# Performance work log

Measured on AMD Instinct MI355X. Metric: run time of the kernel, lower is better.

The kernel has to match this reference:

```python
import jax, jax.numpy as jnp
import numpy as np

N_HEAD, D_MODEL, D_HEAD = 16, 1024, 64
QLEN, BSZ, RLEN = 2048, 2, 2048
SCALE = 1.0 / (D_HEAD ** 0.5)


def setup_inputs() -> dict:
    key = jax.random.key(0)
    ks = jax.random.split(key, 7)
    return {
        "w": jax.random.normal(ks[0], (QLEN, BSZ, D_MODEL), dtype=jnp.float32),
        "r": jax.random.normal(ks[1], (RLEN, D_MODEL), dtype=jnp.float32),
        "qkv_w": jax.random.normal(ks[2], (D_MODEL, 3 * N_HEAD * D_HEAD), dtype=jnp.float32) * 0.02,
        "r_net_w": jax.random.normal(ks[3], (D_MODEL, N_HEAD * D_HEAD), dtype=jnp.float32) * 0.02,
        "o_w": jax.random.normal(ks[4], (N_HEAD * D_HEAD, D_MODEL), dtype=jnp.float32) * 0.02,
        "r_r_bias": jax.random.normal(ks[5], (N_HEAD, D_HEAD), dtype=jnp.float32) * 0.02,
        "r_w_bias": jax.random.normal(ks[6], (N_HEAD, D_HEAD), dtype=jnp.float32) * 0.02,
    }


def _rel_shift(x):
    # x: [qlen, rlen, bsz, n_head]
    q, r, b, n = x.shape
    x = jnp.pad(x, ((0, 0), (1, 0), (0, 0), (0, 0)))
    x = x.reshape(r + 1, q, b, n)[1:]
    return x.reshape(q, r, b, n)


def reference(w, r, qkv_w, r_net_w, o_w, r_r_bias, r_w_bias):
    qlen, bsz, _ = w.shape
    rlen = r.shape[0]
    # qkv projection: [qlen, bsz, 3*H*D]
    w_heads = jnp.einsum('ibm,mh->ibh', w, qkv_w)
    w_head_q, w_head_k, w_head_v = jnp.split(w_heads, 3, axis=-1)
    klen = w_head_k.shape[0]
    w_head_q = w_head_q.reshape(qlen, bsz, N_HEAD, D_HEAD)
    w_head_k = w_head_k.reshape(klen, bsz, N_HEAD, D_HEAD)
    w_head_v = w_head_v.reshape(klen, bsz, N_HEAD, D_HEAD)
    # relative position keys: [rlen, H, D]
    r_head_k = jnp.einsum('jm,mh->jh', r, r_net_w).reshape(rlen, N_HEAD, D_HEAD)

    rw_head_q = w_head_q + r_w_bias  # content bias
    rr_head_q = w_head_q + r_r_bias  # position bias
    AC = jnp.einsum('ibnd,jbnd->ijbn', rw_head_q, w_head_k)
    BD = jnp.einsum('ibnd,jnd->ijbn', rr_head_q, r_head_k)
    BD = _rel_shift(BD)[:, :klen]

    attn_score = (AC + BD) * SCALE
    attn_prob = jax.nn.softmax(attn_score, axis=1)  # over klen axis
    attn_vec = jnp.einsum('ijbn,jbnd->ibnd', attn_prob, w_head_v)
    attn_vec = attn_vec.reshape(qlen, bsz, N_HEAD * D_HEAD)
    attn_out = jnp.einsum('ibh,hm->ibm', attn_vec, o_w)
    return (w + attn_out, attn_prob, AC, BD)
```

## Files before the change

kernel.cpp:

```cpp
#include <hip/hip_runtime.h>
#include <hip/hip_bf16.h>


typedef unsigned short u16;
typedef __attribute__((ext_vector_type(8))) short short8;
typedef __attribute__((ext_vector_type(4))) float f32x4;
typedef __attribute__((ext_vector_type(4))) unsigned short u16x4;

__device__ __forceinline__ u16 f2bf(float x){
  unsigned u = __float_as_uint(x);
  u += 0x7fffu + ((u >> 16) & 1u);
  return (u16)(u >> 16);
}
__device__ __forceinline__ float bf2f(u16 s){
  return __uint_as_float(((unsigned)s) << 16);
}
__device__ __forceinline__ f32x4 mfma16(short8 a, short8 b, f32x4 c){
  return __builtin_amdgcn_mfma_f32_16x16x32_bf16(a, b, c, 0, 0, 0);
}
__device__ __forceinline__ void ntst4(float* p, f32x4 v){
  __builtin_nontemporal_store(v, (f32x4*)p);
}
__device__ __forceinline__ void bar_lds(){
  asm volatile("s_waitcnt lgkmcnt(0)" ::: "memory");
  __builtin_amdgcn_s_barrier();
}


__global__ __launch_bounds__(256) void k_cast(const float* __restrict__ src, u16* __restrict__ dst, int n4){
  int i = blockIdx.x * 256 + threadIdx.x;
  if (i >= n4) return;
  f32x4 v = *(const f32x4*)(src + (size_t)i * 4);
  u16x4 o;
  #pragma unroll
  for (int q = 0; q < 4; ++q) o[q] = f2bf(v[q]);
  *(u16x4*)(dst + (size_t)i * 4) = o;
}

__global__ __launch_bounds__(256) void k_tc(const float* __restrict__ src, u16* __restrict__ dst, int R, int C){
  __shared__ float ld[32][33];
  int c0 = blockIdx.x * 32, r0 = blockIdx.y * 32;
  int t = threadIdx.x;
  int r = t >> 3, c4 = (t & 7) * 4;
  f32x4 v = *(const f32x4*)(src + (size_t)(r0 + r) * C + c0 + c4);
  #pragma unroll
  for (int q = 0; q < 4; ++q) ld[r][c4 + q] = v[q];
  __syncthreads();
  int c = t >> 3, r4 = (t & 7) * 4;
  u16x4 o;
  #pragma unroll
  for (int q = 0; q < 4; ++q) o[q] = f2bf(ld[r4 + q][c]);
  *(u16x4*)(dst + (size_t)(c0 + c) * R + r0 + r4) = o;
}


template<int MODE>
__global__ __launch_bounds__(512) void k_gemm(const u16* __restrict__ A, const u16* __restrict__ Bt,
        u16* __restrict__ o0, u16* __restrict__ o1, u16* __restrict__ o2,
        const float* __restrict__ wres, float* __restrict__ outf)
{
  __shared__ __align__(16) u16 As[128][40];
  __shared__ __align__(16) u16 Bs[256][40];
  const int t = threadIdx.x;
  const int wave = t >> 6, lane = t & 63;
  const int wr = wave >> 2, wc = wave & 3;
  const int g = lane >> 4, li = lane & 15;
  const int m0 = blockIdx.x * 128, n0 = blockIdx.y * 256;
  f32x4 acc[4][4] = {};
  const int ar = t >> 2, ac8 = (t & 3) * 8;
  for (int kt = 0; kt < 32; ++kt){
    int k0 = kt * 32;
    *(short8*)&As[ar][ac8] = *(const short8*)(A + (size_t)(m0 + ar) * 1024 + k0 + ac8);
    #pragma unroll
    for (int u = 0; u < 2; ++u){
      int id = t + 512 * u; int br = id >> 2, bc8 = (id & 3) * 8;
      *(short8*)&Bs[br][bc8] = *(const short8*)(Bt + (size_t)(n0 + br) * 1024 + k0 + bc8);
    }
    bar_lds();
    short8 af[4], bfv[4];
    #pragma unroll
    for (int mf = 0; mf < 4; ++mf) af[mf] = *(const short8*)&As[wr * 64 + mf * 16 + li][g * 8];
    #pragma unroll
    for (int nf = 0; nf < 4; ++nf) bfv[nf] = *(const short8*)&Bs[wc * 64 + nf * 16 + li][g * 8];
    #pragma unroll
    for (int mf = 0; mf < 4; ++mf)
      #pragma unroll
      for (int nf = 0; nf < 4; ++nf)
        acc[mf][nf] = mfma16(af[mf], bfv[nf], acc[mf][nf]);
    bar_lds();
  }
  #pragma unroll
  for (int mf = 0; mf < 4; ++mf)
  #pragma unroll
  for (int nf = 0; nf < 4; ++nf)
  #pragma unroll
  for (int r = 0; r < 4; ++r){
    int gr = m0 + wr * 64 + mf * 16 + g * 4 + r;
    int gc = n0 + wc * 64 + nf * 16 + li;
    float v = acc[mf][nf][r];
    if (MODE == 0){
      int part = gc >> 10, hh = gc & 1023;
      int hn = hh >> 6, d = hh & 63;
      int i = gr >> 1, b = gr & 1;
      u16* dst = (part == 0) ? o0 : ((part == 1) ? o1 : o2);
      dst[((((b << 4) + hn) * 2048 + i) << 6) + d] = f2bf(v);
    } else if (MODE == 1){
      int hn = gc >> 6, d = gc & 63;
      o0[((hn * 2048 + gr) << 6) + d] = f2bf(v);
    } else {
      size_t idx = (size_t)gr * 1024 + gc;
      outf[idx] = wres[idx] + v;
    }
  }
}

__global__ __launch_bounds__(256) void k_bias(const u16* __restrict__ Km, const float* __restrict__ bv,
                                              float* __restrict__ out, int total){
  int idx = blockIdx.x * 256 + threadIdx.x;
  if (idx >= total) return;
  int n = (idx >> 11) & 15;
  const u16* kr = Km + ((size_t)idx << 6);
  const float* bp = bv + n * 64;
  float s = 0.f;
  #pragma unroll
  for (int d8 = 0; d8 < 8; ++d8){
    short8 v = *(const short8*)(kr + d8 * 8);
    #pragma unroll
    for (int q = 0; q < 8; ++q) s += bp[d8 * 8 + q] * bf2f((u16)v[q]);
  }
  out[idx] = s;
}

__global__ __launch_bounds__(256) void k_trv(const u16* __restrict__ V, u16* __restrict__ Vt){
  __shared__ __align__(16) u16 ld[64][72];
  int bn = blockIdx.x, j0 = blockIdx.y * 64;
  int t = threadIdx.x;
  #pragma unroll
  for (int u = 0; u < 2; ++u){
    int id = t + 256 * u; int r = id >> 3, c8 = (id & 7) * 8;
    *(short8*)&ld[r][c8] = *(const short8*)(V + ((size_t)(bn * 2048 + j0 + r) << 6) + c8);
  }
  __syncthreads();
  #pragma unroll
  for (int u = 0; u < 2; ++u){
    int id = t + 256 * u; int d = id >> 3, j8 = (id & 7) * 8;
    short8 o;
    #pragma unroll
    for (int q = 0; q < 8; ++q) o[q] = ld[j8 + q][d];
    *(short8*)(Vt + ((size_t)(bn * 64 + d) << 11) + j0 + j8) = o;
  }
}

template<typename F>
__device__ __forceinline__ void ring_step(int ch, int m, F&& do_tile){
  if (ch == 0){
    do_tile(m + 2032, false);
    do_tile(m - 32, true);
    do_tile(m - 16, true);
  }
  do_tile(m + 2048, false);
  do_tile(m + 2064, false);
  do_tile(m, true);
  do_tile(m + 16, true);
}

__global__ __launch_bounds__(512, 4) void k_statsR(const u16* __restrict__ Q, const u16* __restrict__ RK,
        const u16* __restrict__ Kc, const float* __restrict__ bias_ac, const float* __restrict__ bias_bd,
        float* __restrict__ ACo, float* __restrict__ BDo,
        float* __restrict__ m_part, float* __restrict__ l_part)
{
  __shared__ u16 sBD[2][16 * 544];
  __shared__ u16 sB[32 * 271];
  const int t = threadIdx.x, wave = t >> 6, lane = t & 63;
  const int g = lane >> 4, li = lane & 15;
  const int i0 = blockIdx.x * 16, b = blockIdx.y;
  const int jbase = blockIdx.z * 512;
  short8 qa[2][2], qb[2][2];
  #pragma unroll
  for (int nn = 0; nn < 2; ++nn){
    int bn = b * 16 + wave * 2 + nn;
    const u16* qp = Q + ((size_t)(bn * 2048 + i0 + li) << 6) + g * 8;
    qa[nn][0] = *(const short8*)qp;
    qa[nn][1] = *(const short8*)(qp + 32);
    int rowB = i0 + 1 + li; if (rowB > 2047) rowB = 2047;
    const u16* qp2 = Q + ((size_t)(bn * 2048 + rowB) << 6) + g * 8;
    qb[nn][0] = *(const short8*)qp2;
    qb[nn][1] = *(const short8*)(qp2 + 32);
  }
  for (int w2 = t; w2 < 2 * 4352; w2 += 512) ((unsigned*)sBD)[w2] = 0;

  float m_[2][4], l_[2][4];
  #pragma unroll
  for (int nn = 0; nn < 2; ++nn)
    #pragma unroll
    for (int r = 0; r < 4; ++r){ m_[nn][r] = -__builtin_inff(); l_[nn][r] = 0.f; }

  int cur = 0;
  for (int ch = 0; ch < 16; ++ch){
    int j0 = jbase + ch * 32;
    int m = j0 - i0;
    bar_lds();
    u16* bufA = &sBD[cur][0];
    u16* bufB = &sBD[cur ^ 1][0];

    auto do_tile = [&](int c0, bool case2){
      if (c0 < 0 || c0 > 2032) return;
      int off = c0 - m + (case2 ? 2 : -2047);
      #pragma unroll
      for (int nn = 0; nn < 2; ++nn){
        int n = wave * 2 + nn;
        const u16* rp = RK + ((size_t)(n * 2048 + c0 + li) << 6) + g * 8;
        short8 b0 = *(const short8*)rp;
        short8 b1 = *(const short8*)(rp + 32);
        f32x4 acc = {};
        acc = mfma16(case2 ? qb[nn][0] : qa[nn][0], b0, acc);
        acc = mfma16(case2 ? qb[nn][1] : qa[nn][1], b1, acc);
        float bb = bias_bd[n * 2048 + c0 + li];
        #pragma unroll
        for (int r = 0; r < 4; ++r){
          int fr = g * 4 + r;
          int jw = li + fr + off;
          u16 val = f2bf(acc[r] + bb);
          if ((unsigned)jw < 32u)       bufA[fr * 544 + jw * 17 + n] = val;
          else if ((unsigned)jw < 64u)  bufB[fr * 544 + (jw - 32) * 17 + n] = val;
        }
      }
    };
    ring_step(ch, m, do_tile);
    bar_lds();

    #pragma unroll
    for (int nn = 0; nn < 2; ++nn){
      int n = wave * 2 + nn, bn = b * 16 + n;
      float sv[2][4];
      #pragma unroll
      for (int cf = 0; cf < 2; ++cf){
        int jc = j0 + cf * 16 + li;
        const u16* kp = Kc + ((size_t)(bn * 2048 + jc) << 6) + g * 8;
        short8 b0 = *(const short8*)kp;
        short8 b1 = *(const short8*)(kp + 32);
        f32x4 acc = {};
        acc = mfma16(qa[nn][0], b0, acc);
        acc = mfma16(qa[nn][1], b1, acc);
        float ba = bias_ac[bn * 2048 + jc];
        #pragma unroll
        for (int r = 0; r < 4; ++r){
          float av = acc[r] + ba;
          sB[(cf * 16 + li) * 271 + n * 17 + g * 4 + r] = f2bf(av);
          float bd = bf2f(bufA[(g * 4 + r) * 544 + (cf * 16 + li) * 17 + n]);
          sv[cf][r] = (av + bd) * 0.125f;
        }
      }
      float cm[4], mn[4], ps[4];
      #pragma unroll
      for (int r = 0; r < 4; ++r) cm[r] = fmaxf(sv[0][r], sv[1][r]);
      #pragma unroll
      for (int off = 1; off < 16; off <<= 1)
        #pragma unroll
        for (int r = 0; r < 4; ++r) cm[r] = fmaxf(cm[r], __shfl_xor(cm[r], off));
      #pragma unroll
      for (int r = 0; r < 4; ++r){
        mn[r] = fmaxf(m_[nn][r], cm[r]);
        ps[r] = __expf(sv[0][r] - mn[r]) + __expf(sv[1][r] - mn[r]);
      }
      #pragma unroll
      for (int off = 1; off < 16; off <<= 1)
        #pragma unroll
        for (int r = 0; r < 4; ++r) ps[r] += __shfl_xor(ps[r], off);
      #pragma unroll
      for (int r = 0; r < 4; ++r){
        l_[nn][r] = l_[nn][r] * __expf(m_[nn][r] - mn[r]) + ps[r];
        m_[nn][r] = mn[r];
      }
    }
    #pragma unroll
    for (int u = 0; u < 4; ++u){
      int flat4 = t + 512 * u;
      int n4 = (flat4 & 3) * 4, jl = (flat4 >> 2) & 31, row = flat4 >> 7;
      f32x4 v;
      #pragma unroll
      for (int q = 0; q < 4; ++q) v[q] = bf2f(bufA[row * 544 + jl * 17 + n4 + q]);
      ntst4(BDo + (((size_t)(i0 + row) * 2048 + j0 + jl) << 5) + b * 16 + n4, v);
    }
    bar_lds();
    #pragma unroll
    for (int u = 0; u < 4; ++u){
      int flat4 = t + 512 * u;
      int n4 = (flat4 & 3) * 4, jl = (flat4 >> 2) & 31, row = flat4 >> 7;
      f32x4 v;
      #pragma unroll
      for (int q = 0; q < 4; ++q) v[q] = bf2f(sB[jl * 271 + (n4 + q) * 17 + row]);
      ntst4(ACo + (((size_t)(i0 + row) * 2048 + j0 + jl) << 5) + b * 16 + n4, v);
    }
    for (int w2 = t; w2 < 4352; w2 += 512) ((unsigned*)bufA)[w2] = 0;
    cur ^= 1;
  }
  if (li == 0){
    #pragma unroll
    for (int nn = 0; nn < 2; ++nn)
      #pragma unroll
      for (int r = 0; r < 4; ++r){
        int bn = b * 16 + wave * 2 + nn;
        size_t o = ((size_t)(blockIdx.z * 32 + bn)) * 2048 + i0 + g * 4 + r;
        m_part[o] = m_[nn][r];
        l_part[o] = l_[nn][r];
      }
  }
}

__global__ __launch_bounds__(256) void k_comb(const float* __restrict__ mp, const float* __restrict__ lp,
                                              float* __restrict__ mf, float* __restrict__ lf){
  int idx = blockIdx.x * 256 + threadIdx.x;
  float m = -__builtin_inff();
  #pragma unroll
  for (int js = 0; js < 4; ++js) m = fmaxf(m, mp[js * 65536 + idx]);
  float l = 0.f;
  #pragma unroll
  for (int js = 0; js < 4; ++js) l += lp[js * 65536 + idx] * __expf(mp[js * 65536 + idx] - m);
  mf[idx] = m;
  lf[idx] = l;
}

__global__ __launch_bounds__(512, 4) void k_prob_pv(const u16* __restrict__ Q, const u16* __restrict__ Kc,
        const u16* __restrict__ Vt, const float* __restrict__ bias_ac, const float* __restrict__ BD,
        const float* __restrict__ m_f, const float* __restrict__ l_f,
        float* __restrict__ PROB, float* __restrict__ Ovp)
{
  __shared__ __align__(16) u16 sA[16 * 648];
  __shared__ u16 sB[32 * 271];
  const int t = threadIdx.x, wave = t >> 6, lane = t & 63;
  const int g = lane >> 4, li = lane & 15;
  const int i0 = blockIdx.x * 16, b = blockIdx.y;
  const int jbase = blockIdx.z * 512;
  short8 qa[2][2];
  float m_[2][4], rl_[2][4];
  #pragma unroll
  for (int nn = 0; nn < 2; ++nn){
    int bn = b * 16 + wave * 2 + nn;
    const u16* qp = Q + ((size_t)(bn * 2048 + i0 + li) << 6) + g * 8;
    qa[nn][0] = *(const short8*)qp;
    qa[nn][1] = *(const short8*)(qp + 32);
    #pragma unroll
    for (int r = 0; r < 4; ++r){
      m_[nn][r]  = m_f[bn * 2048 + i0 + g * 4 + r];
      rl_[nn][r] = 1.f / l_f[bn * 2048 + i0 + g * 4 + r];
    }
  }
  f32x4 oacc[2][4] = {};

  f32x4 pfv[4];
  #pragma unroll
  for (int u = 0; u < 4; ++u){
    int flat4 = t + 512 * u;
    int n4 = (flat4 & 3) * 4, jl = (flat4 >> 2) & 31, row = flat4 >> 7;
    pfv[u] = *(const f32x4*)(BD + (((size_t)(i0 + row) * 2048 + jbase + jl) << 5) + b * 16 + n4);
  }

  for (int ch = 0; ch < 16; ++ch){
    int j0 = jbase + ch * 32;
    bar_lds();
    #pragma unroll
    for (int u = 0; u < 4; ++u){
      int flat4 = t + 512 * u;
      int n4 = (flat4 & 3) * 4, jl = (flat4 >> 2) & 31, row = flat4 >> 7;
      u16x4 o;
      #pragma unroll
      for (int q = 0; q < 4; ++q) o[q] = (u16)(__float_as_uint(pfv[u][q]) >> 16);
      *(u16x4*)&sA[row * 648 + jl * 20 + n4] = o;
    }
    if (ch + 1 < 16){
      #pragma unroll
      for (int u = 0; u < 4; ++u){
        int flat4 = t + 512 * u;
        int n4 = (flat4 & 3) * 4, jl = (flat4 >> 2) & 31, row = flat4 >> 7;
        pfv[u] = *(const f32x4*)(BD + (((size_t)(i0 + row) * 2048 + j0 + 32 + jl) << 5) + b * 16 + n4);
      }
    }
    bar_lds();
    #pragma unroll
    for (int nn = 0; nn < 2; ++nn){
      int n = wave * 2 + nn, bn = b * 16 + n;
      #pragma unroll
      for (int cf = 0; cf < 2; ++cf){
        int jc = j0 + cf * 16 + li;
        const u16* kp = Kc + ((size_t)(bn * 2048 + jc) << 6) + g * 8;
        short8 b0 = *(const short8*)kp;
        short8 b1 = *(const short8*)(kp + 32);
        f32x4 acc = {};
        acc = mfma16(qa[nn][0], b0, acc);
        acc = mfma16(qa[nn][1], b1, acc);
        float ba = bias_ac[bn * 2048 + jc];
        #pragma unroll
        for (int r = 0; r < 4; ++r){
          float bd = bf2f(sA[(g * 4 + r) * 648 + (cf * 16 + li) * 20 + n]);
          float s = (acc[r] + ba + bd) * 0.125f;
          float p = __expf(s - m_[nn][r]) * rl_[nn][r];
          sB[(cf * 16 + li) * 271 + n * 17 + g * 4 + r] = f2bf(p);
        }
      }
    }
    #pragma unroll
    for (int nn = 0; nn < 2; ++nn){
      int n = wave * 2 + nn, bn = b * 16 + n;
      short8 pa;
      #pragma unroll
      for (int tt = 0; tt < 8; ++tt) pa[tt] = (short)sB[(g * 8 + tt) * 271 + n * 17 + li];
      const u16* vb = Vt + ((size_t)(bn * 64) << 11) + j0 + g * 8;
      #pragma unroll
      for (int vf = 0; vf < 4; ++vf){
        short8 bv = *(const short8*)(vb + ((size_t)(vf * 16 + li) << 11));
        oacc[nn][vf] = mfma16(pa, bv, oacc[nn][vf]);
      }
    }
    bar_lds();
    #pragma unroll
    for (int u = 0; u < 4; ++u){
      int flat4 = t + 512 * u;
      int n4 = (flat4 & 3) * 4, jl = (flat4 >> 2) & 31, row = flat4 >> 7;
      f32x4 v;
      #pragma unroll
      for (int q = 0; q < 4; ++q) v[q] = bf2f(sB[jl * 271 + (n4 + q) * 17 + row]);
      ntst4(PROB + (((size_t)(i0 + row) * 2048 + j0 + jl) << 5) + b * 16 + n4, v);
    }
  }
  float* op = Ovp + (size_t)blockIdx.z * 4194304;
  #pragma unroll
  for (int nn = 0; nn < 2; ++nn){
    int n = wave * 2 + nn;
    #pragma unroll
    for (int vf = 0; vf < 4; ++vf)
      #pragma unroll
      for (int r = 0; r < 4; ++r)
        op[(size_t)((i0 + g * 4 + r) * 2 + b) * 1024 + n * 64 + vf * 16 + li] = oacc[nn][vf][r];
  }
}

__global__ __launch_bounds__(256) void k_ovred(const float* __restrict__ ovp, u16* __restrict__ ov){
  int i = blockIdx.x * 256 + threadIdx.x;
  const f32x4* p = (const f32x4*)ovp;
  f32x4 s = p[i];
  #pragma unroll
  for (int js = 1; js < 4; ++js) s += p[(size_t)js * 1048576 + i];
  u16x4 o;
  #pragma unroll
  for (int q = 0; q < 4; ++q) o[q] = f2bf(s[q]);
  ((u16x4*)ov)[i] = o;
}


extern "C" void kernel_launch(void* const* d_in, const int* in_sizes, int n_in,
                              void* d_out, int out_size, void* d_ws, size_t ws_size,
                              hipStream_t stream)
{
  const float* w      = (const float*)d_in[0];
  const float* r      = (const float*)d_in[1];
  const float* qkv_w  = (const float*)d_in[2];
  const float* rnet_w = (const float*)d_in[3];
  const float* o_w    = (const float*)d_in[4];
  const float* rrb    = (const float*)d_in[5];
  const float* rwb    = (const float*)d_in[6];

  char* ws = (char*)d_ws;
  size_t off = 0;
  auto alloc = [&](size_t bytes) -> void* {
    void* p = ws + off; off += (bytes + 255) & ~(size_t)255; return p;
  };
  u16* Xbf    = (u16*)alloc((size_t)4096 * 1024 * 2);
  u16* Rbf    = (u16*)alloc((size_t)2048 * 1024 * 2);
  u16* Wqkvt  = (u16*)alloc((size_t)3072 * 1024 * 2);
  u16* Wrt    = (u16*)alloc((size_t)1024 * 1024 * 2);
  u16* Wot    = (u16*)alloc((size_t)1024 * 1024 * 2);
  u16* Qs     = (u16*)alloc((size_t)32 * 2048 * 64 * 2);
  u16* Ks     = (u16*)alloc((size_t)32 * 2048 * 64 * 2);
  u16* Vs     = (u16*)alloc((size_t)32 * 2048 * 64 * 2);
  u16* Vts    = (u16*)alloc((size_t)32 * 64 * 2048 * 2);
  u16* RKs    = (u16*)alloc((size_t)16 * 2048 * 64 * 2);
  float* bias_ac = (float*)alloc((size_t)32 * 2048 * 4);
  float* bias_bd = (float*)alloc((size_t)16 * 2048 * 4);
  float* m_part  = (float*)alloc((size_t)4 * 32 * 2048 * 4);
  float* l_part  = (float*)alloc((size_t)4 * 32 * 2048 * 4);
  float* m_fin   = (float*)alloc((size_t)32 * 2048 * 4);
  float* l_fin   = (float*)alloc((size_t)32 * 2048 * 4);
  float* Ovp     = (float*)alloc((size_t)4 * 4096 * 1024 * 4);
  u16* Ov     = (u16*)alloc((size_t)4096 * 1024 * 2);

  float* out0 = (float*)d_out;
  float* PROB = out0 + 4194304;
  float* ACo  = PROB + 134217728;
  float* BDo  = ACo  + 134217728;

  k_cast<<<dim3(4096), dim3(256), 0, stream>>>(w, Xbf, 1048576);
  k_cast<<<dim3(2048), dim3(256), 0, stream>>>(r, Rbf, 524288);
  k_tc<<<dim3(96, 32), dim3(256), 0, stream>>>(qkv_w,  Wqkvt, 1024, 3072);
  k_tc<<<dim3(32, 32), dim3(256), 0, stream>>>(rnet_w, Wrt,   1024, 1024);
  k_tc<<<dim3(32, 32), dim3(256), 0, stream>>>(o_w,    Wot,   1024, 1024);
  k_gemm<0><<<dim3(32, 12), dim3(512), 0, stream>>>(Xbf, Wqkvt, Qs, Ks, Vs, nullptr, nullptr);
  k_gemm<1><<<dim3(16, 4),  dim3(512), 0, stream>>>(Rbf, Wrt,  RKs, nullptr, nullptr, nullptr, nullptr);
  k_bias<<<dim3(256), dim3(256), 0, stream>>>(Ks,  rwb, bias_ac, 65536);
  k_bias<<<dim3(128), dim3(256), 0, stream>>>(RKs, rrb, bias_bd, 32768);
  k_trv<<<dim3(32, 32), dim3(256), 0, stream>>>(Vs, Vts);
  k_statsR<<<dim3(128, 2, 4), dim3(512), 0, stream>>>(Qs, RKs, Ks, bias_ac, bias_bd, ACo, BDo, m_part, l_part);
  k_comb<<<dim3(256), dim3(256), 0, stream>>>(m_part, l_part, m_fin, l_fin);
  k_prob_pv<<<dim3(128, 2, 4), dim3(512), 0, stream>>>(Qs, Ks, Vts, bias_ac, BDo, m_fin, l_fin, PROB, Ovp);
  k_ovred<<<dim3(4096), dim3(256), 0, stream>>>(Ovp, Ov);
  k_gemm<2><<<dim3(32, 4), dim3(512), 0, stream>>>(Ov, Wot, nullptr, nullptr, nullptr, w, out0);
}
```

Baseline: 1.243 ms.

## Recompute BD in prob pass instead of rereading it, swap MFMA operands

The probability/PV kernel now recomputes the relative-position BD scores through the same ring-buffered MFMA scheme as the stats kernel, instead of reading the fp32 BD output back from global memory. Both kernels swap MFMA operand order so each lane holds one query row, which turns per-row softmax reductions into scalar values with two cross-lane shuffles. They also use vectorized bias loads, an XOR-swizzled LDS layout and packed P fragments built straight from registers. This trades a large global read for extra MFMA work and LDS ring maintenance in the second pass.

```diff
diff --git a/kernel.cpp b/kernel.cpp
--- a/kernel.cpp
+++ b/kernel.cpp
@@ -4,6 +4,7 @@
 
 typedef unsigned short u16;
 typedef __attribute__((ext_vector_type(8))) short short8;
+typedef __attribute__((ext_vector_type(4))) short s16x4;
 typedef __attribute__((ext_vector_type(4))) float f32x4;
 typedef __attribute__((ext_vector_type(4))) unsigned short u16x4;
 
@@ -24,6 +25,9 @@
 __device__ __forceinline__ void bar_lds(){
   asm volatile("s_waitcnt lgkmcnt(0)" ::: "memory");
   __builtin_amdgcn_s_barrier();
+}
+__device__ __forceinline__ int ridx(int il, int k, int n){
+  return (((il * 8 + k) << 4) + n) ^ (il & 15);
 }
 
 
@@ -76,7 +80,7 @@
       int id = t + 512 * u; int br = id >> 2, bc8 = (id & 3) * 8;
       *(short8*)&Bs[br][bc8] = *(const short8*)(Bt + (size_t)(n0 + br) * 1024 + k0 + bc8);
     }
-    bar_lds();
+    __syncthreads();
     short8 af[4], bfv[4];
     #pragma unroll
     for (int mf = 0; mf < 4; ++mf) af[mf] = *(const short8*)&As[wr * 64 + mf * 16 + li][g * 8];
@@ -87,7 +91,7 @@
       #pragma unroll
       for (int nf = 0; nf < 4; ++nf)
         acc[mf][nf] = mfma16(af[mf], bfv[nf], acc[mf][nf]);
-    bar_lds();
+    __syncthreads();
   }
   #pragma unroll
   for (int mf = 0; mf < 4; ++mf)
@@ -169,8 +173,8 @@
         float* __restrict__ ACo, float* __restrict__ BDo,
         float* __restrict__ m_part, float* __restrict__ l_part)
 {
-  __shared__ u16 sBD[2][16 * 544];
-  __shared__ u16 sB[32 * 271];
+  __shared__ __align__(16) u16 sRing[2][8192];
+  __shared__ __align__(16) u16 sAC[8192];
   const int t = threadIdx.x, wave = t >> 6, lane = t & 63;
   const int g = lane >> 4, li = lane & 15;
   const int i0 = blockIdx.x * 16, b = blockIdx.y;
@@ -187,21 +191,19 @@
     qb[nn][0] = *(const short8*)qp2;
     qb[nn][1] = *(const short8*)(qp2 + 32);
   }
-  for (int w2 = t; w2 < 2 * 4352; w2 += 512) ((unsigned*)sBD)[w2] = 0;
-
-  float m_[2][4], l_[2][4];
-  #pragma unroll
-  for (int nn = 0; nn < 2; ++nn)
-    #pragma unroll
-    for (int r = 0; r < 4; ++r){ m_[nn][r] = -__builtin_inff(); l_[nn][r] = 0.f; }
+  for (int w2 = t; w2 < 8192; w2 += 512) ((unsigned*)sRing)[w2] = 0;
+
+  float m_[2], l_[2];
+  #pragma unroll
+  for (int nn = 0; nn < 2; ++nn){ m_[nn] = -__builtin_inff(); l_[nn] = 0.f; }
 
   int cur = 0;
   for (int ch = 0; ch < 16; ++ch){
     int j0 = jbase + ch * 32;
     int m = j0 - i0;
     bar_lds();
-    u16* bufA = &sBD[cur][0];
-    u16* bufB = &sBD[cur ^ 1][0];
+    u16* bufA = &sRing[cur][0];
+    u16* bufB = &sRing[cur ^ 1][0];
 
     auto do_tile = [&](int c0, bool case2){
       if (c0 < 0 || c0 > 2032) return;
@@ -213,16 +215,15 @@
         short8 b0 = *(const short8*)rp;
         short8 b1 = *(const short8*)(rp + 32);
         f32x4 acc = {};
-        acc = mfma16(case2 ? qb[nn][0] : qa[nn][0], b0, acc);
-        acc = mfma16(case2 ? qb[nn][1] : qa[nn][1], b1, acc);
-        float bb = bias_bd[n * 2048 + c0 + li];
+        acc = mfma16(b0, case2 ? qb[nn][0] : qa[nn][0], acc);
+        acc = mfma16(b1, case2 ? qb[nn][1] : qa[nn][1], acc);
+        f32x4 bb4 = *(const f32x4*)(bias_bd + n * 2048 + c0 + g * 4);
         #pragma unroll
         for (int r = 0; r < 4; ++r){
-          int fr = g * 4 + r;
-          int jw = li + fr + off;
-          u16 val = f2bf(acc[r] + bb);
-          if ((unsigned)jw < 32u)       bufA[fr * 544 + jw * 17 + n] = val;
-          else if ((unsigned)jw < 64u)  bufB[fr * 544 + (jw - 32) * 17 + n] = val;
+          int jw = li + g * 4 + r + off;
+          u16 val = f2bf(acc[r] + bb4[r]);
+          if ((unsigned)jw < 32u)       bufA[ridx(li, jw >> 2, n) * 4 + (jw & 3)] = val;
+          else if ((unsigned)jw < 64u){ int j2 = jw - 32; bufB[ridx(li, j2 >> 2, n) * 4 + (j2 & 3)] = val; }
         }
       }
     };
@@ -235,43 +236,37 @@
       float sv[2][4];
       #pragma unroll
       for (int cf = 0; cf < 2; ++cf){
-        int jc = j0 + cf * 16 + li;
-        const u16* kp = Kc + ((size_t)(bn * 2048 + jc) << 6) + g * 8;
+        const u16* kp = Kc + ((size_t)(bn * 2048 + j0 + cf * 16 + li) << 6) + g * 8;
         short8 b0 = *(const short8*)kp;
         short8 b1 = *(const short8*)(kp + 32);
         f32x4 acc = {};
-        acc = mfma16(qa[nn][0], b0, acc);
-        acc = mfma16(qa[nn][1], b1, acc);
-        float ba = bias_ac[bn * 2048 + jc];
+        acc = mfma16(b0, qa[nn][0], acc);
+        acc = mfma16(b1, qa[nn][1], acc);
+        f32x4 ba4 = *(const f32x4*)(bias_ac + bn * 2048 + j0 + cf * 16 + g * 4);
+        u16x4 bdq = *((const u16x4*)bufA + ridx(li, cf * 4 + g, n));
+        u16x4 acq;
         #pragma unroll
         for (int r = 0; r < 4; ++r){
-          float av = acc[r] + ba;
-          sB[(cf * 16 + li) * 271 + n * 17 + g * 4 + r] = f2bf(av);
-          float bd = bf2f(bufA[(g * 4 + r) * 544 + (cf * 16 + li) * 17 + n]);
-          sv[cf][r] = (av + bd) * 0.125f;
+          float av = acc[r] + ba4[r];
+          acq[r] = f2bf(av);
+          sv[cf][r] = (av + bf2f(bdq[r])) * 0.125f;
         }
+        *((u16x4*)sAC + ridx(li, cf * 4 + g, n)) = acq;
       }
-      float cm[4], mn[4], ps[4];
-      #pragma unroll
-      for (int r = 0; r < 4; ++r) cm[r] = fmaxf(sv[0][r], sv[1][r]);
-      #pragma unroll
-      for (int off = 1; off < 16; off <<= 1)
+      float cm = fmaxf(fmaxf(fmaxf(sv[0][0], sv[0][1]), fmaxf(sv[0][2], sv[0][3])),
+                       fmaxf(fmaxf(sv[1][0], sv[1][1]), fmaxf(sv[1][2], sv[1][3])));
+      cm = fmaxf(cm, __shfl_xor(cm, 16));
+      cm = fmaxf(cm, __shfl_xor(cm, 32));
+      float mn = fmaxf(m_[nn], cm);
+      float ps = 0.f;
+      #pragma unroll
+      for (int cf = 0; cf < 2; ++cf)
         #pragma unroll
-        for (int r = 0; r < 4; ++r) cm[r] = fmaxf(cm[r], __shfl_xor(cm[r], off));
-      #pragma unroll
-      for (int r = 0; r < 4; ++r){
-        mn[r] = fmaxf(m_[nn][r], cm[r]);
-        ps[r] = __expf(sv[0][r] - mn[r]) + __expf(sv[1][r] - mn[r]);
-      }
-      #pragma unroll
-      for (int off = 1; off < 16; off <<= 1)
-        #pragma unroll
-        for (int r = 0; r < 4; ++r) ps[r] += __shfl_xor(ps[r], off);
-      #pragma unroll
-      for (int r = 0; r < 4; ++r){
-        l_[nn][r] = l_[nn][r] * __expf(m_[nn][r] - mn[r]) + ps[r];
-        m_[nn][r] = mn[r];
-      }
+        for (int r = 0; r < 4; ++r) ps += __expf(sv[cf][r] - mn);
+      ps += __shfl_xor(ps, 16);
+      ps += __shfl_xor(ps, 32);
+      l_[nn] = l_[nn] * __expf(m_[nn] - mn) + ps;
+      m_[nn] = mn;
     }
     #pragma unroll
     for (int u = 0; u < 4; ++u){
@@ -279,7 +274,7 @@
       int n4 = (flat4 & 3) * 4, jl = (flat4 >> 2) & 31, row = flat4 >> 7;
       f32x4 v;
       #pragma unroll
-      for (int q = 0; q < 4; ++q) v[q] = bf2f(bufA[row * 544 + jl * 17 + n4 + q]);
+      for (int q = 0; q < 4; ++q) v[q] = bf2f(bufA[ridx(row, jl >> 2, n4 + q) * 4 + (jl & 3)]);
       ntst4(BDo + (((size_t)(i0 + row) * 2048 + j0 + jl) << 5) + b * 16 + n4, v);
     }
     bar_lds();
@@ -289,22 +284,20 @@
       int n4 = (flat4 & 3) * 4, jl = (flat4 >> 2) & 31, row = flat4 >> 7;
       f32x4 v;
       #pragma unroll
-      for (int q = 0; q < 4; ++q) v[q] = bf2f(sB[jl * 271 + (n4 + q) * 17 + row]);
+      for (int q = 0; q < 4; ++q) v[q] = bf2f(sAC[ridx(row, jl >> 2, n4 + q) * 4 + (jl & 3)]);
       ntst4(ACo + (((size_t)(i0 + row) * 2048 + j0 + jl) << 5) + b * 16 + n4, v);
     }
-    for (int w2 = t; w2 < 4352; w2 += 512) ((unsigned*)bufA)[w2] = 0;
+    for (int w2 = t; w2 < 4096; w2 += 512) ((unsigned*)bufA)[w2] = 0;
     cur ^= 1;
   }
-  if (li == 0){
-    #pragma unroll
-    for (int nn = 0; nn < 2; ++nn)
-      #pragma unroll
-      for (int r = 0; r < 4; ++r){
-        int bn = b * 16 + wave * 2 + nn;
-        size_t o = ((size_t)(blockIdx.z * 32 + bn)) * 2048 + i0 + g * 4 + r;
-        m_part[o] = m_[nn][r];
-        l_part[o] = l_[nn][r];
-      }
+  if (lane < 16){
+    #pragma unroll
+    for (int nn = 0; nn < 2; ++nn){
+      int bn = b * 16 + wave * 2 + nn;
+      size_t o = ((size_t)(blockIdx.z * 32 + bn)) * 2048 + i0 + li;
+      m_part[o] = m_[nn];
+      l_part[o] = l_[nn];
+    }
   }
 }
 
@@ -321,94 +314,104 @@
   lf[idx] = l;
 }
 
-__global__ __launch_bounds__(512, 4) void k_prob_pv(const u16* __restrict__ Q, const u16* __restrict__ Kc,
-        const u16* __restrict__ Vt, const float* __restrict__ bias_ac, const float* __restrict__ BD,
+__global__ __launch_bounds__(512, 4) void k_prob_pv(const u16* __restrict__ Q, const u16* __restrict__ RK,
+        const u16* __restrict__ Kc, const u16* __restrict__ Vt,
+        const float* __restrict__ bias_ac, const float* __restrict__ bias_bd,
         const float* __restrict__ m_f, const float* __restrict__ l_f,
         float* __restrict__ PROB, float* __restrict__ Ovp)
 {
-  __shared__ __align__(16) u16 sA[16 * 648];
-  __shared__ u16 sB[32 * 271];
+  __shared__ __align__(16) u16 sRing[2][8192];
+  __shared__ __align__(16) u16 sP[8192];
   const int t = threadIdx.x, wave = t >> 6, lane = t & 63;
   const int g = lane >> 4, li = lane & 15;
   const int i0 = blockIdx.x * 16, b = blockIdx.y;
   const int jbase = blockIdx.z * 512;
   short8 qa[2][2];
-  float m_[2][4], rl_[2][4];
+  float m_[2], rl_[2];
   #pragma unroll
   for (int nn = 0; nn < 2; ++nn){
     int bn = b * 16 + wave * 2 + nn;
     const u16* qp = Q + ((size_t)(bn * 2048 + i0 + li) << 6) + g * 8;
     qa[nn][0] = *(const short8*)qp;
     qa[nn][1] = *(const short8*)(qp + 32);
-    #pragma unroll
-    for (int r = 0; r < 4; ++r){
-      m_[nn][r]  = m_f[bn * 2048 + i0 + g * 4 + r];
-      rl_[nn][r] = 1.f / l_f[bn * 2048 + i0 + g * 4 + r];
-    }
-  }
+    m_[nn]  = m_f[bn * 2048 + i0 + li];
+    rl_[nn] = 1.f / l_f[bn * 2048 + i0 + li];
+  }
+  for (int w2 = t; w2 < 8192; w2 += 512) ((unsigned*)sRing)[w2] = 0;
   f32x4 oacc[2][4] = {};
 
-  f32x4 pfv[4];
-  #pragma unroll
-  for (int u = 0; u < 4; ++u){
-    int flat4 = t + 512 * u;
-    int n4 = (flat4 & 3) * 4, jl = (flat4 >> 2) & 31, row = flat4 >> 7;
-    pfv[u] = *(const f32x4*)(BD + (((size_t)(i0 + row) * 2048 + jbase + jl) << 5) + b * 16 + n4);
-  }
-
+  int cur = 0;
   for (int ch = 0; ch < 16; ++ch){
     int j0 = jbase + ch * 32;
+    int m = j0 - i0;
     bar_lds();
-    #pragma unroll
-    for (int u = 0; u < 4; ++u){
-      int flat4 = t + 512 * u;
-      int n4 = (flat4 & 3) * 4, jl = (flat4 >> 2) & 31, row = flat4 >> 7;
-      u16x4 o;
-      #pragma unroll
-      for (int q = 0; q < 4; ++q) o[q] = (u16)(__float_as_uint(pfv[u][q]) >> 16);
-      *(u16x4*)&sA[row * 648 + jl * 20 + n4] = o;
-    }
-    if (ch + 1 < 16){
-      #pragma unroll
-      for (int u = 0; u < 4; ++u){
-        int flat4 = t + 512 * u;
-        int n4 = (flat4 & 3) * 4, jl = (flat4 >> 2) & 31, row = flat4 >> 7;
-        pfv[u] = *(const f32x4*)(BD + (((size_t)(i0 + row) * 2048 + j0 + 32 + jl) << 5) + b * 16 + n4);
+    u16* bufA = &sRing[cur][0];
+    u16* bufB = &sRing[cur ^ 1][0];
+    {
+      short8 qb[2][2];
+      #pragma unroll
+      for (int nn = 0; nn < 2; ++nn){
+        int bn = b * 16 + wave * 2 + nn;
+        int rowB = i0 + 1 + li; if (rowB > 2047) rowB = 2047;
+        const u16* qp2 = Q + ((size_t)(bn * 2048 + rowB) << 6) + g * 8;
+        qb[nn][0] = *(const short8*)qp2;
+        qb[nn][1] = *(const short8*)(qp2 + 32);
       }
+      auto do_tile = [&](int c0, bool case2){
+        if (c0 < 0 || c0 > 2032) return;
+        int off = c0 - m + (case2 ? 2 : -2047);
+        #pragma unroll
+        for (int nn = 0; nn < 2; ++nn){
+          int n = wave * 2 + nn;
+          const u16* rp = RK + ((size_t)(n * 2048 + c0 + li) << 6) + g * 8;
+          short8 b0 = *(const short8*)rp;
+          short8 b1 = *(const short8*)(rp + 32);
+          f32x4 acc = {};
+          acc = mfma16(b0, case2 ? qb[nn][0] : qa[nn][0], acc);
+          acc = mfma16(b1, case2 ? qb[nn][1] : qa[nn][1], acc);
+          f32x4 bb4 = *(const f32x4*)(bias_bd + n * 2048 + c0 + g * 4);
+          #pragma unroll
+          for (int r = 0; r < 4; ++r){
+            int jw = li + g * 4 + r + off;
+            u16 val = f2bf(acc[r] + bb4[r]);
+            if ((unsigned)jw < 32u)       bufA[ridx(li, jw >> 2, n) * 4 + (jw & 3)] = val;
+            else if ((unsigned)jw < 64u){ int j2 = jw - 32; bufB[ridx(li, j2 >> 2, n) * 4 + (j2 & 3)] = val; }
+          }
+        }
+      };
+      ring_step(ch, m, do_tile);
     }
     bar_lds();
+
     #pragma unroll
     for (int nn = 0; nn < 2; ++nn){
       int n = wave * 2 + nn, bn = b * 16 + n;
+      s16x4 pq[2];
       #pragma unroll
       for (int cf = 0; cf < 2; ++cf){
-        int jc = j0 + cf * 16 + li;
-        const u16* kp = Kc + ((size_t)(bn * 2048 + jc) << 6) + g * 8;
+        const u16* kp = Kc + ((size_t)(bn * 2048 + j0 + cf * 16 + li) << 6) + g * 8;
         short8 b0 = *(const short8*)kp;
         short8 b1 = *(const short8*)(kp + 32);
         f32x4 acc = {};
-        acc = mfma16(qa[nn][0], b0, acc);
-        acc = mfma16(qa[nn][1], b1, acc);
-        float ba = bias_ac[bn * 2048 + jc];
+        acc = mfma16(b0, qa[nn][0], acc);
+        acc = mfma16(b1, qa[nn][1], acc);
+        f32x4 ba4 = *(const f32x4*)(bias_ac + bn * 2048 + j0 + cf * 16 + g * 4);
+        u16x4 bdq = *((const u16x4*)bufA + ridx(li, cf * 4 + g, n));
         #pragma unroll
         for (int r = 0; r < 4; ++r){
-          float bd = bf2f(sA[(g * 4 + r) * 648 + (cf * 16 + li) * 20 + n]);
-          float s = (acc[r] + ba + bd) * 0.125f;
-          float p = __expf(s - m_[nn][r]) * rl_[nn][r];
-          sB[(cf * 16 + li) * 271 + n * 17 + g * 4 + r] = f2bf(p);
+          float s = (acc[r] + ba4[r] + bf2f(bdq[r])) * 0.125f;
+          float p = __expf(s - m_[nn]) * rl_[nn];
+          pq[cf][r] = (short)f2bf(p);
         }
+        *((s16x4*)sP + ridx(li, cf * 4 + g, n)) = pq[cf];
       }
-    }
-    #pragma unroll
-    for (int nn = 0; nn < 2; ++nn){
-      int n = wave * 2 + nn, bn = b * 16 + n;
-      short8 pa;
-      #pragma unroll
-      for (int tt = 0; tt < 8; ++tt) pa[tt] = (short)sB[(g * 8 + tt) * 271 + n * 17 + li];
-      const u16* vb = Vt + ((size_t)(bn * 64) << 11) + j0 + g * 8;
+      short8 pa = __builtin_shufflevector(pq[0], pq[1], 0, 1, 2, 3, 4, 5, 6, 7);
       #pragma unroll
       for (int vf = 0; vf < 4; ++vf){
-        short8 bv = *(const short8*)(vb + ((size_t)(vf * 16 + li) << 11));
+        const u16* vp = Vt + ((size_t)(bn * 64 + vf * 16 + li) << 11) + j0 + g * 4;
+        s16x4 v0 = *(const s16x4*)vp;
+        s16x4 v1 = *(const s16x4*)(vp + 16);
+        short8 bv = __builtin_shufflevector(v0, v1, 0, 1, 2, 3, 4, 5, 6, 7);
         oacc[nn][vf] = mfma16(pa, bv, oacc[nn][vf]);
       }
     }
@@ -419,9 +422,11 @@
       int n4 = (flat4 & 3) * 4, jl = (flat4 >> 2) & 31, row = flat4 >> 7;
       f32x4 v;
       #pragma unroll
-      for (int q = 0; q < 4; ++q) v[q] = bf2f(sB[jl * 271 + (n4 + q) * 17 + row]);
+      for (int q = 0; q < 4; ++q) v[q] = bf2f(sP[ridx(row, jl >> 2, n4 + q) * 4 + (jl & 3)]);
       ntst4(PROB + (((size_t)(i0 + row) * 2048 + j0 + jl) << 5) + b * 16 + n4, v);
     }
+    for (int w2 = t; w2 < 4096; w2 += 512) ((unsigned*)bufA)[w2] = 0;
+    cur ^= 1;
   }
   float* op = Ovp + (size_t)blockIdx.z * 4194304;
   #pragma unroll
@@ -501,7 +506,7 @@
   k_trv<<<dim3(32, 32), dim3(256), 0, stream>>>(Vs, Vts);
   k_statsR<<<dim3(128, 2, 4), dim3(512), 0, stream>>>(Qs, RKs, Ks, bias_ac, bias_bd, ACo, BDo, m_part, l_part);
   k_comb<<<dim3(256), dim3(256), 0, stream>>>(m_part, l_part, m_fin, l_fin);
-  k_prob_pv<<<dim3(128, 2, 4), dim3(512), 0, stream>>>(Qs, Ks, Vts, bias_ac, BDo, m_fin, l_fin, PROB, Ovp);
+  k_prob_pv<<<dim3(128, 2, 4), dim3(512), 0, stream>>>(Qs, RKs, Ks, Vts, bias_ac, bias_bd, m_fin, l_fin, PROB, Ovp);
   k_ovred<<<dim3(4096), dim3(256), 0, stream>>>(Ovp, Ov);
   k_gemm<2><<<dim3(32, 4), dim3(512), 0, stream>>>(Ov, Wot, nullptr, nullptr, nullptr, w, out0);
 }
```

After: 1.596 ms. 1.28x slower.
